# Kernel tuning notes

Measured on AMD Instinct MI355X. Metric: run time of the kernel, lower is better.

## Reference

```python
import jax, jax.numpy as jnp
import numpy as np

N = 40000
E = 640000
D_RNA = 1000
D_PROT = 300
H = 64      # hidden_channels
OUT = 32    # out_channels
HEADS = 4


def setup_inputs() -> dict:
    key = jax.random.key(0)
    ks = jax.random.split(key, 24)
    s = 0.05
    w = lambda k, shape: jax.random.normal(k, shape, jnp.float32) * s
    inp = {
        'x': jax.random.normal(ks[0], (N, D_RNA + D_PROT), jnp.float32),
        'edge_index': jax.random.randint(ks[1], (2, E), 0, N, jnp.int32),
        'input_dim_rna': D_RNA,
        # embeddings
        'W_rna': w(ks[2], (D_RNA, H)), 'b_rna': jnp.zeros((H,), jnp.float32),
        'W_prot': w(ks[3], (D_PROT, H)), 'b_prot': jnp.zeros((H,), jnp.float32),
        # GATConv1: in 2H=128 -> heads*H=256
        'W1s': w(ks[4], (2 * H, HEADS * H)), 'W1d': w(ks[5], (2 * H, HEADS * H)),
        'att1_s': w(ks[6], (HEADS, H)), 'att1_d': w(ks[7], (HEADS, H)),
        'bias1': jnp.zeros((HEADS * H,), jnp.float32),
        # lin1: 2H -> heads*H
        'Wl1': w(ks[8], (2 * H, HEADS * H)), 'bl1': jnp.zeros((HEADS * H,), jnp.float32),
        # GATConv2: in heads*H=256 -> heads*OUT=128
        'W2s': w(ks[9], (HEADS * H, HEADS * OUT)), 'W2d': w(ks[10], (HEADS * H, HEADS * OUT)),
        'att2_s': w(ks[11], (HEADS, OUT)), 'att2_d': w(ks[12], (HEADS, OUT)),
        'bias2': jnp.zeros((HEADS * OUT,), jnp.float32),
        # lin2: heads*H -> heads*OUT
        'Wl2': w(ks[13], (HEADS * H, HEADS * OUT)), 'bl2': jnp.zeros((HEADS * OUT,), jnp.float32),
    }
    return inp


def _gat(x_in, edge_index, Ws, Wd, att_s, att_d, bias, heads, ch):
    # PyG GATConv, bipartite weights, add_self_loops=False, concat=True, eval (no dropout)
    n = x_in.shape[0]
    src, dst = edge_index[0], edge_index[1]
    xs = (x_in @ Ws).reshape(n, heads, ch)   # source projection
    xd = (x_in @ Wd).reshape(n, heads, ch)   # destination projection
    a_s = jnp.einsum('nhc,hc->nh', xs, att_s)  # [N,H]
    a_d = jnp.einsum('nhc,hc->nh', xd, att_d)  # [N,H]
    e = jax.nn.leaky_relu(a_s[src] + a_d[dst], 0.2)          # [E,H]
    m = jax.lax.stop_gradient(jax.ops.segment_max(e, dst, num_segments=n))
    p = jnp.exp(e - m[dst])
    denom = jax.ops.segment_sum(p, dst, num_segments=n)       # [N,H]
    alpha = p / denom[dst]                                    # segment softmax over incoming edges
    msg = xs[src] * alpha[:, :, None]                         # [E,H,C]
    agg = jax.ops.segment_sum(msg, dst, num_segments=n)       # [N,H,C]
    return agg.reshape(n, heads * ch) + bias


def reference(x, edge_index, input_dim_rna, W_rna, b_rna, W_prot, b_prot,
              W1s, W1d, att1_s, att1_d, bias1, Wl1, bl1,
              W2s, W2d, att2_s, att2_d, bias2, Wl2, bl2):
    x_rna = x[:, :input_dim_rna] @ W_rna + b_rna
    x_prot = x[:, input_dim_rna:] @ W_prot + b_prot
    h = jnp.concatenate([x_rna, x_prot], axis=1)              # [N, 2H]
    h = _gat(h, edge_index, W1s, W1d, att1_s, att1_d, bias1, HEADS, H) + h @ Wl1 + bl1
    h = jax.nn.relu(h)
    out = _gat(h, edge_index, W2s, W2d, att2_s, att2_d, bias2, HEADS, OUT) + h @ Wl2 + bl2
    return out
```

## Files before the change

### kernel.cpp

```cpp
#include <hip/hip_runtime.h>
#include <hip/hip_bf16.h>
#include <stdint.h>


#define HEADS 4
#define CH1   64
#define CH2   32
#define HC1   256
#define HC2   128

static constexpr int D_RNA  = 1000;
static constexpr int D_PROT = 300;
static constexpr int D_IN   = 1300;
static constexpr int HDIM   = 128;

typedef __bf16 bf16x8 __attribute__((ext_vector_type(8)));
typedef float  f32x4  __attribute__((ext_vector_type(4)));
typedef unsigned short ushort;

__device__ __forceinline__ float lrelu(float x) { return x >= 0.f ? x : 0.2f * x; }
__device__ __forceinline__ float bf2f(unsigned int u16) {
  return __uint_as_float(u16 << 16);
}
__device__ __forceinline__ ushort f2bf(float f) {
  union { float f; unsigned int u; } x; x.f = f;
  unsigned int r = x.u + 0x7fffu + ((x.u >> 16) & 1u);
  return (ushort)(r >> 16);
}

__global__ void zero_i32(int* p, int n) {
  int i = blockIdx.x * 256 + threadIdx.x;
  if (i < n) p[i] = 0;
}

__global__ void hist_kernel(const int* __restrict__ dstv, int* __restrict__ deg, int E) {
  int i = blockIdx.x * 256 + threadIdx.x;
  if (i < E) atomicAdd(&deg[dstv[i]], 1);
}

__global__ void scan_kernel(const int* __restrict__ deg, int* __restrict__ off,
                            int* __restrict__ cur, int n) {
  __shared__ int s[1024];
  int tid = threadIdx.x;
  const int CHK = (n + 1023) / 1024;
  int base = tid * CHK;
  int sum = 0;
  for (int j = 0; j < CHK; ++j) {
    int i = base + j;
    if (i < n) sum += deg[i];
  }
  s[tid] = sum;
  __syncthreads();
  for (int o = 1; o < 1024; o <<= 1) {
    int t = (tid >= o) ? s[tid - o] : 0;
    __syncthreads();
    s[tid] += t;
    __syncthreads();
  }
  int run = s[tid] - sum;
  for (int j = 0; j < CHK; ++j) {
    int i = base + j;
    if (i < n) {
      off[i] = run; cur[i] = run;
      run += deg[i];
    }
  }
  if (tid == 1023) off[n] = s[1023];
}

__global__ void scatter_kernel(const int* __restrict__ srcv, const int* __restrict__ dstv,
                               int* __restrict__ cur, int* __restrict__ srcs, int E) {
  int i = blockIdx.x * 256 + threadIdx.x;
  if (i < E) {
    int d = dstv[i];
    int pos = atomicAdd(&cur[d], 1);
    srcs[pos] = srcv[i];
  }
}

__global__ void fold_att_kernel(const float* __restrict__ W1s, const float* __restrict__ W1d,
                                const float* __restrict__ at1s, const float* __restrict__ at1d,
                                const float* __restrict__ W2s, const float* __restrict__ W2d,
                                const float* __restrict__ at2s, const float* __restrict__ at2d,
                                float* v1s, float* v1d, float* v2s, float* v2d) {
  int tid = blockIdx.x * blockDim.x + threadIdx.x;
  int stride = gridDim.x * blockDim.x;
  for (int o = tid; o < HDIM * HEADS; o += stride) {
    int k = o >> 2, h = o & 3;
    float ss = 0.f, sd = 0.f;
    for (int c = 0; c < CH1; ++c) {
      ss += W1s[k * HC1 + h * CH1 + c] * at1s[h * CH1 + c];
      sd += W1d[k * HC1 + h * CH1 + c] * at1d[h * CH1 + c];
    }
    v1s[o] = ss; v1d[o] = sd;
  }
  for (int o = tid; o < HC1 * HEADS; o += stride) {
    int k = o >> 2, h = o & 3;
    float ss = 0.f, sd = 0.f;
    for (int c = 0; c < CH2; ++c) {
      ss += W2s[k * HC2 + h * CH2 + c] * at2s[h * CH2 + c];
      sd += W2d[k * HC2 + h * CH2 + c] * at2d[h * CH2 + c];
    }
    v2s[o] = ss; v2d[o] = sd;
  }
}

__global__ void convert_weights(const float* __restrict__ W_rna, const float* __restrict__ W_prot,
                                const float* __restrict__ W1s, const float* __restrict__ Wl1,
                                const float* __restrict__ W2s, const float* __restrict__ Wl2,
                                const float* __restrict__ b1, const float* __restrict__ bl1,
                                const float* __restrict__ b2, const float* __restrict__ bl2,
                                ushort* BTr, ushort* BTp, ushort* BT1, ushort* BT2,
                                float* biasL1, float* biasL2) {
  int tid = blockIdx.x * blockDim.x + threadIdx.x;
  int stride = gridDim.x * blockDim.x;
  for (int i = tid; i < 64 * 1024; i += stride) {
    int n = i >> 10, k = i & 1023;
    BTr[i] = (k < D_RNA) ? f2bf(W_rna[k * 64 + n]) : 0;
  }
  for (int i = tid; i < 64 * 320; i += stride) {
    int n = i / 320, k = i - n * 320;
    BTp[i] = (k < D_PROT) ? f2bf(W_prot[k * 64 + n]) : 0;
  }
  for (int i = tid; i < 512 * 128; i += stride) {
    int n = i >> 7, k = i & 127;
    BT1[i] = f2bf(n < 256 ? W1s[k * 256 + n] : Wl1[k * 256 + n - 256]);
  }
  for (int i = tid; i < 256 * 256; i += stride) {
    int n = i >> 8, k = i & 255;
    BT2[i] = f2bf(n < 128 ? W2s[k * 128 + n] : Wl2[k * 128 + n - 128]);
  }
  for (int i = tid; i < 512; i += stride) biasL1[i] = (i < 256) ? b1[i] : bl1[i - 256];
  for (int i = tid; i < 256; i += stride) biasL2[i] = (i < 128) ? b2[i] : bl2[i - 128];
}

#define LDK 72

__device__ __forceinline__ f32x4 mfma_bf16(bf16x8 a, bf16x8 b, f32x4 c) {
  return __builtin_amdgcn_mfma_f32_16x16x32_bf16(a, b, c, 0, 0, 0);
}

__launch_bounds__(256)
__global__ void embed_gemm(const float* __restrict__ x,
                           const ushort* __restrict__ BTr, const ushort* __restrict__ BTp,
                           const float* __restrict__ b_rna, const float* __restrict__ b_prot,
                           ushort* __restrict__ h0) {
  const bool prot = (blockIdx.x == 1);
  const int Kpad = prot ? 320 : 1024;
  const int acol = prot ? D_RNA : 0;
  const ushort* BT = prot ? BTp : BTr;
  const float* bias = prot ? b_prot : b_rna;
  const int r0 = blockIdx.y * 64;

  __shared__ ushort As[64 * LDK];
  __shared__ ushort Bs[64 * LDK];
  int tid = threadIdx.x;
  int wave = tid >> 6, lane = tid & 63;
  int quad = lane >> 4, lr = lane & 15;
  f32x4 acc[4];
#pragma unroll
  for (int c = 0; c < 4; ++c) acc[c] = (f32x4){0.f, 0.f, 0.f, 0.f};

  int srow = tid >> 2, skq = (tid & 3) * 16;
  const float* aprow = x + (size_t)(r0 + srow) * D_IN;
  const ushort* bprow = BT + (size_t)srow * Kpad;

  float4 fa[4];
  uint4 fb0, fb1;

  auto loadA = [&](int k0) {
#pragma unroll
    for (int q = 0; q < 4; ++q) {
      int kg = acol + k0 + skq + q * 4;
      fa[q] = (kg + 4 <= D_IN) ? *(const float4*)(aprow + kg)
                               : make_float4(0.f, 0.f, 0.f, 0.f);
    }
  };
  auto loadB = [&](int k0) {
    const ushort* bp = bprow + k0 + skq;
    fb0 = *(const uint4*)bp;
    fb1 = *(const uint4*)(bp + 8);
  };

  loadA(0);
  loadB(0);

  for (int k0 = 0; k0 < Kpad; k0 += 64) {
    {
      ushort tmp[16];
#pragma unroll
      for (int q = 0; q < 4; ++q) {
        tmp[q * 4 + 0] = f2bf(fa[q].x); tmp[q * 4 + 1] = f2bf(fa[q].y);
        tmp[q * 4 + 2] = f2bf(fa[q].z); tmp[q * 4 + 3] = f2bf(fa[q].w);
      }
      *(uint4*)&As[srow * LDK + skq] = *(const uint4*)&tmp[0];
      *(uint4*)&As[srow * LDK + skq + 8] = *(const uint4*)&tmp[8];
      *(uint4*)&Bs[srow * LDK + skq] = fb0;
      *(uint4*)&Bs[srow * LDK + skq + 8] = fb1;
    }
    __syncthreads();
    if (k0 + 64 < Kpad) {
      loadA(k0 + 64);
      loadB(k0 + 64);
    }
    int arow = wave * 16 + lr;
    bf16x8 a0 = *(const bf16x8*)&As[arow * LDK + quad * 8];
    bf16x8 a1 = *(const bf16x8*)&As[arow * LDK + 32 + quad * 8];
#pragma unroll
    for (int c = 0; c < 4; ++c) {
      bf16x8 b0 = *(const bf16x8*)&Bs[(c * 16 + lr) * LDK + quad * 8];
      bf16x8 b1 = *(const bf16x8*)&Bs[(c * 16 + lr) * LDK + 32 + quad * 8];
      acc[c] = mfma_bf16(a0, b0, acc[c]);
      acc[c] = mfma_bf16(a1, b1, acc[c]);
    }
    __syncthreads();
  }
  int colb = prot ? 64 : 0;
#pragma unroll
  for (int c = 0; c < 4; ++c) {
#pragma unroll
    for (int j = 0; j < 4; ++j) {
      int row = r0 + wave * 16 + quad * 4 + j;
      int col = c * 16 + lr;
      h0[(size_t)row * HDIM + colb + col] = f2bf(acc[c][j] + bias[col]);
    }
  }
}

__launch_bounds__(256)
__global__ void layer_gemm(const ushort* __restrict__ A, int K,
                           const ushort* __restrict__ BT, const float* __restrict__ bias,
                           ushort* __restrict__ out0, ushort* __restrict__ out1, int halfw) {
  const int cb = blockIdx.x * 64;
  const int r0 = blockIdx.y * 64;
  __shared__ ushort As[64 * LDK];
  __shared__ ushort Bs[64 * LDK];
  int tid = threadIdx.x;
  int wave = tid >> 6, lane = tid & 63;
  int quad = lane >> 4, lr = lane & 15;
  f32x4 acc[4];
#pragma unroll
  for (int c = 0; c < 4; ++c) acc[c] = (f32x4){0.f, 0.f, 0.f, 0.f};

  int srow = tid >> 2, skq = (tid & 3) * 16;
  const ushort* aprow = A + (size_t)(r0 + srow) * K;
  const ushort* bprow = BT + (size_t)(cb + srow) * K;

  uint4 fa0, fa1, fb0, fb1;
  auto loadAB = [&](int k0) {
    const ushort* ap = aprow + k0 + skq;
    const ushort* bp = bprow + k0 + skq;
    fa0 = *(const uint4*)ap;
    fa1 = *(const uint4*)(ap + 8);
    fb0 = *(const uint4*)bp;
    fb1 = *(const uint4*)(bp + 8);
  };

  loadAB(0);

  for (int k0 = 0; k0 < K; k0 += 64) {
    *(uint4*)&As[srow * LDK + skq] = fa0;
    *(uint4*)&As[srow * LDK + skq + 8] = fa1;
    *(uint4*)&Bs[srow * LDK + skq] = fb0;
    *(uint4*)&Bs[srow * LDK + skq + 8] = fb1;
    __syncthreads();
    if (k0 + 64 < K) loadAB(k0 + 64);
    int arow = wave * 16 + lr;
    bf16x8 a0 = *(const bf16x8*)&As[arow * LDK + quad * 8];
    bf16x8 a1 = *(const bf16x8*)&As[arow * LDK + 32 + quad * 8];
#pragma unroll
    for (int c = 0; c < 4; ++c) {
      bf16x8 b0 = *(const bf16x8*)&Bs[(c * 16 + lr) * LDK + quad * 8];
      bf16x8 b1 = *(const bf16x8*)&Bs[(c * 16 + lr) * LDK + 32 + quad * 8];
      acc[c] = mfma_bf16(a0, b0, acc[c]);
      acc[c] = mfma_bf16(a1, b1, acc[c]);
    }
    __syncthreads();
  }
#pragma unroll
  for (int c = 0; c < 4; ++c) {
#pragma unroll
    for (int j = 0; j < 4; ++j) {
      int row = r0 + wave * 16 + quad * 4 + j;
      int cg = cb + c * 16 + lr;
      ushort v = f2bf(acc[c][j] + bias[cg]);
      if (cg < halfw) out0[(size_t)row * halfw + cg] = v;
      else            out1[(size_t)row * halfw + cg - halfw] = v;
    }
  }
}

__launch_bounds__(256)
__global__ void attn_proj_kernel(const ushort* __restrict__ h, int K,
                                 const float* __restrict__ vs, const float* __restrict__ vd,
                                 float* __restrict__ a_s, float* __restrict__ a_d, int N) {
  extern __shared__ float lds[];
  float* VsT = lds;
  float* VdT = lds + 4 * K;
  for (int idx = threadIdx.x; idx < 4 * K; idx += 256) {
    int j = idx / K, k = idx - j * K;
    VsT[j * K + k] = vs[k * 4 + j];
    VdT[j * K + k] = vd[k * 4 + j];
  }
  __syncthreads();
  int wave = threadIdx.x >> 6, lane = threadIdx.x & 63;
  int n = blockIdx.x * 4 + wave;
  if (n >= N) return;
  float as[4] = {0.f, 0.f, 0.f, 0.f}, ad[4] = {0.f, 0.f, 0.f, 0.f};
  const ushort* hp = h + (size_t)n * K;
  for (int k = lane; k < K; k += 64) {
    float hv = bf2f(hp[k]);
#pragma unroll
    for (int j = 0; j < 4; ++j) {
      as[j] += hv * VsT[j * K + k];
      ad[j] += hv * VdT[j * K + k];
    }
  }
#pragma unroll
  for (int j = 0; j < 4; ++j) {
    for (int o = 32; o; o >>= 1) {
      as[j] += __shfl_xor(as[j], o);
      ad[j] += __shfl_xor(ad[j], o);
    }
  }
  if (lane == 0) {
#pragma unroll
    for (int j = 0; j < 4; ++j) {
      a_s[(size_t)n * 4 + j] = as[j];
      a_d[(size_t)n * 4 + j] = ad[j];
    }
  }
}

__launch_bounds__(256)
__global__ void edge_softmax_kernel(const int* __restrict__ off, const int* __restrict__ srcs,
                                    const float* __restrict__ a_s, const float* __restrict__ a_d,
                                    float* __restrict__ alpha, float* __restrict__ rden, int N) {
  int lane = threadIdx.x & 63;
  int wave = threadIdx.x >> 6;
  int g = lane >> 4, l = lane & 15;
  int n = (blockIdx.x * 4 + wave) * 4 + g;
  if (n >= N) return;
  int s0 = off[n], s1 = off[n + 1];
  float4 ad = *(const float4*)&a_d[(size_t)n * 4];
  float mx = -1e30f, my = -1e30f, mz = -1e30f, mw = -1e30f;
  for (int i = s0 + l; i < s1; i += 16) {
    float4 as = *(const float4*)&a_s[(size_t)srcs[i] * 4];
    mx = fmaxf(mx, lrelu(as.x + ad.x));
    my = fmaxf(my, lrelu(as.y + ad.y));
    mz = fmaxf(mz, lrelu(as.z + ad.z));
    mw = fmaxf(mw, lrelu(as.w + ad.w));
  }
#pragma unroll
  for (int o = 1; o < 16; o <<= 1) {
    mx = fmaxf(mx, __shfl_xor(mx, o));
    my = fmaxf(my, __shfl_xor(my, o));
    mz = fmaxf(mz, __shfl_xor(mz, o));
    mw = fmaxf(mw, __shfl_xor(mw, o));
  }
  float sx = 0.f, sy = 0.f, sz = 0.f, sw = 0.f;
  for (int i = s0 + l; i < s1; i += 16) {
    float4 as = *(const float4*)&a_s[(size_t)srcs[i] * 4];
    float4 p;
    p.x = expf(lrelu(as.x + ad.x) - mx);
    p.y = expf(lrelu(as.y + ad.y) - my);
    p.z = expf(lrelu(as.z + ad.z) - mz);
    p.w = expf(lrelu(as.w + ad.w) - mw);
    sx += p.x; sy += p.y; sz += p.z; sw += p.w;
    *(float4*)&alpha[(size_t)i * 4] = p;
  }
#pragma unroll
  for (int o = 1; o < 16; o <<= 1) {
    sx += __shfl_xor(sx, o);
    sy += __shfl_xor(sy, o);
    sz += __shfl_xor(sz, o);
    sw += __shfl_xor(sw, o);
  }
  if (l == 0) {
    float4 r;
    r.x = sx > 0.f ? 1.f / sx : 0.f;
    r.y = sy > 0.f ? 1.f / sy : 0.f;
    r.z = sz > 0.f ? 1.f / sz : 0.f;
    r.w = sw > 0.f ? 1.f / sw : 0.f;
    *(float4*)&rden[(size_t)n * 4] = r;
  }
}

template <int VEC>
__device__ __forceinline__ void load_bf(const ushort* p, float* out);
template <>
__device__ __forceinline__ void load_bf<4>(const ushort* p, float* out) {
  uint2 q = *(const uint2*)p;
  out[0] = bf2f(q.x & 0xffffu); out[1] = bf2f(q.x >> 16);
  out[2] = bf2f(q.y & 0xffffu); out[3] = bf2f(q.y >> 16);
}
template <>
__device__ __forceinline__ void load_bf<2>(const ushort* p, float* out) {
  unsigned int q = *(const unsigned int*)p;
  out[0] = bf2f(q & 0xffffu); out[1] = bf2f(q >> 16);
}

template <int CH, int VEC, bool RELU, bool OUT_BF16>
__launch_bounds__(256)
__global__ void aggregate_kernel(const int* __restrict__ off, const int* __restrict__ srcs,
                                 const float* __restrict__ alpha, const float* __restrict__ rden,
                                 const ushort* __restrict__ xs,
                                 const float* __restrict__ bias,
                                 const ushort* __restrict__ skip,
                                 void* __restrict__ outv, int N) {
  const int HC = 4 * CH;
  int wave = threadIdx.x >> 6, lane = threadIdx.x & 63;
  int n = blockIdx.x * 4 + wave;
  if (n >= N) return;
  int h = lane >> 4;
  int c = (lane & 15) * VEC;
  int i = off[n], end = off[n + 1];
  float acc[VEC];
#pragma unroll
  for (int v = 0; v < VEC; ++v) acc[v] = 0.f;
  for (; i + 2 <= end; i += 2) {
    int sA = srcs[i], sB = srcs[i + 1];
    float wA = alpha[(size_t)i * 4 + h];
    float wB = alpha[(size_t)(i + 1) * 4 + h];
    float xA[VEC], xB[VEC];
    load_bf<VEC>(xs + (size_t)sA * HC + h * CH + c, xA);
    load_bf<VEC>(xs + (size_t)sB * HC + h * CH + c, xB);
#pragma unroll
    for (int v = 0; v < VEC; ++v) acc[v] += wA * xA[v] + wB * xB[v];
  }
  if (i < end) {
    int sA = srcs[i];
    float wA = alpha[(size_t)i * 4 + h];
    float xA[VEC];
    load_bf<VEC>(xs + (size_t)sA * HC + h * CH + c, xA);
#pragma unroll
    for (int v = 0; v < VEC; ++v) acc[v] += wA * xA[v];
  }
  float r = rden[(size_t)n * 4 + h];
  size_t obase = (size_t)n * HC + h * CH + c;
  float sk[VEC];
  load_bf<VEC>(skip + obase, sk);
#pragma unroll
  for (int v = 0; v < VEC; ++v) {
    float val = acc[v] * r + bias[h * CH + c + v] + sk[v];
    if (RELU) val = fmaxf(val, 0.f);
    if (OUT_BF16) ((ushort*)outv)[obase + v] = f2bf(val);
    else          ((float*)outv)[obase + v] = val;
  }
}

extern "C" void kernel_launch(void* const* d_in, const int* in_sizes, int n_in,
                              void* d_out, int out_size, void* d_ws, size_t ws_size,
                              hipStream_t stream) {
  const float* x      = (const float*)d_in[0];
  const int*   ei     = (const int*)d_in[1];
  const float* W_rna  = (const float*)d_in[3];
  const float* b_rna  = (const float*)d_in[4];
  const float* W_prot = (const float*)d_in[5];
  const float* b_prot = (const float*)d_in[6];
  const float* W1s    = (const float*)d_in[7];
  const float* W1d    = (const float*)d_in[8];
  const float* at1s   = (const float*)d_in[9];
  const float* at1d   = (const float*)d_in[10];
  const float* bias1  = (const float*)d_in[11];
  const float* Wl1    = (const float*)d_in[12];
  const float* bl1    = (const float*)d_in[13];
  const float* W2s    = (const float*)d_in[14];
  const float* W2d    = (const float*)d_in[15];
  const float* at2s   = (const float*)d_in[16];
  const float* at2d   = (const float*)d_in[17];
  const float* bias2  = (const float*)d_in[18];
  const float* Wl2    = (const float*)d_in[19];
  const float* bl2    = (const float*)d_in[20];

  const int N = in_sizes[0] / D_IN;
  const int E = in_sizes[1] / 2;
  const int* srcv = ei;
  const int* dstv = ei + E;

  char* ws = (char*)d_ws;
  size_t o = 0;
  auto carve = [&](size_t bytes) {
    void* p = ws + o;
    o += (bytes + 255) & ~(size_t)255;
    return p;
  };
  int* deg    = (int*)carve((size_t)N * 4);
  int* offp   = (int*)carve((size_t)(N + 1) * 4);
  int* cur    = (int*)carve((size_t)N * 4);
  int* srcs   = (int*)carve((size_t)E * 4);
  float* v1s  = (float*)carve(HDIM * HEADS * 4);
  float* v1d  = (float*)carve(HDIM * HEADS * 4);
  float* v2s  = (float*)carve(HC1 * HEADS * 4);
  float* v2d  = (float*)carve(HC1 * HEADS * 4);
  float* a_s  = (float*)carve((size_t)N * 4 * 4);
  float* a_d  = (float*)carve((size_t)N * 4 * 4);
  float* rden = (float*)carve((size_t)N * 4 * 4);
  float* alpha = (float*)carve((size_t)E * 4 * 4);
  ushort* BTr = (ushort*)carve(64 * 1024 * 2);
  ushort* BTp = (ushort*)carve(64 * 320 * 2);
  ushort* BT1 = (ushort*)carve(512 * 128 * 2);
  ushort* BT2 = (ushort*)carve(256 * 256 * 2);
  float* biasL1 = (float*)carve(512 * 4);
  float* biasL2 = (float*)carve(256 * 4);
  ushort* h0  = (ushort*)carve((size_t)N * HDIM * 2);
  ushort* xs1 = (ushort*)carve((size_t)N * HC1 * 2);
  ushort* z1  = (ushort*)carve((size_t)N * HC1 * 2);
  ushort* h1  = (ushort*)carve((size_t)N * HC1 * 2);
  ushort* xs2 = h0;
  ushort* z2  = z1;
  float* out = (float*)d_out;

  zero_i32<<<(N + 255) / 256, 256, 0, stream>>>(deg, N);
  hist_kernel<<<(E + 255) / 256, 256, 0, stream>>>(dstv, deg, E);
  scan_kernel<<<1, 1024, 0, stream>>>(deg, offp, cur, N);
  scatter_kernel<<<(E + 255) / 256, 256, 0, stream>>>(srcv, dstv, cur, srcs, E);
  fold_att_kernel<<<8, 256, 0, stream>>>(W1s, W1d, at1s, at1d, W2s, W2d, at2s, at2d,
                                         v1s, v1d, v2s, v2d);
  convert_weights<<<256, 256, 0, stream>>>(W_rna, W_prot, W1s, Wl1, W2s, Wl2,
                                           bias1, bl1, bias2, bl2,
                                           BTr, BTp, BT1, BT2, biasL1, biasL2);
  embed_gemm<<<dim3(2, N / 64), 256, 0, stream>>>(x, BTr, BTp, b_rna, b_prot, h0);
  layer_gemm<<<dim3(8, N / 64), 256, 0, stream>>>(h0, HDIM, BT1, biasL1, xs1, z1, HC1);
  attn_proj_kernel<<<N / 4, 256, 8 * HDIM * 4, stream>>>(h0, HDIM, v1s, v1d, a_s, a_d, N);
  edge_softmax_kernel<<<N / 16, 256, 0, stream>>>(offp, srcs, a_s, a_d, alpha, rden, N);
  aggregate_kernel<CH1, 4, true, true><<<N / 4, 256, 0, stream>>>(offp, srcs, alpha, rden, xs1,
                                                                  bias1, z1, h1, N);
  layer_gemm<<<dim3(4, N / 64), 256, 0, stream>>>(h1, HC1, BT2, biasL2, xs2, z2, HC2);
  attn_proj_kernel<<<N / 4, 256, 8 * HC1 * 4, stream>>>(h1, HC1, v2s, v2d, a_s, a_d, N);
  edge_softmax_kernel<<<N / 16, 256, 0, stream>>>(offp, srcs, a_s, a_d, alpha, rden, N);
  aggregate_kernel<CH2, 2, false, false><<<N / 4, 256, 0, stream>>>(offp, srcs, alpha, rden, xs2,
                                                                    bias2, z2, out, N);
}
```

Baseline: 762.1 us.

## Split RNA embedding GEMM along K and widen K tile to 128

The RNA embedding GEMM is split into two K-halves computed by separate blocks, and their fp32 partial sums go to a workspace buffer. A new reduce kernel adds the halves plus bias into h0. The K step per iteration grows from 64 to 128, with the protein weights padded to 384. This balances work between the RNA and protein blocks and halves the number of barriers, at the cost of an extra launch, more shared memory per block and an extra fp32 round trip of about 20MB.

```diff
diff --git a/kernel.cpp b/kernel.cpp
--- a/kernel.cpp
+++ b/kernel.cpp
@@ -118,8 +118,8 @@
     int n = i >> 10, k = i & 1023;
     BTr[i] = (k < D_RNA) ? f2bf(W_rna[k * 64 + n]) : 0;
   }
-  for (int i = tid; i < 64 * 320; i += stride) {
-    int n = i / 320, k = i - n * 320;
+  for (int i = tid; i < 64 * 384; i += stride) {
+    int n = i / 384, k = i - n * 384;
     BTp[i] = (k < D_PROT) ? f2bf(W_prot[k * 64 + n]) : 0;
   }
   for (int i = tid; i < 512 * 128; i += stride) {
@@ -134,7 +134,8 @@
   for (int i = tid; i < 256; i += stride) biasL2[i] = (i < 128) ? b2[i] : bl2[i - 128];
 }
 
-#define LDK 72
+#define LDK  72
+#define LDKE 136
 
 __device__ __forceinline__ f32x4 mfma_bf16(bf16x8 a, bf16x8 b, f32x4 c) {
   return __builtin_amdgcn_mfma_f32_16x16x32_bf16(a, b, c, 0, 0, 0);
@@ -143,17 +144,20 @@
 __launch_bounds__(256)
 __global__ void embed_gemm(const float* __restrict__ x,
                            const ushort* __restrict__ BTr, const ushort* __restrict__ BTp,
-                           const float* __restrict__ b_rna, const float* __restrict__ b_prot,
-                           ushort* __restrict__ h0) {
-  const bool prot = (blockIdx.x == 1);
-  const int Kpad = prot ? 320 : 1024;
-  const int acol = prot ? D_RNA : 0;
-  const ushort* BT = prot ? BTp : BTr;
-  const float* bias = prot ? b_prot : b_rna;
+                           const float* __restrict__ b_prot,
+                           float* __restrict__ Ppart,
+                           ushort* __restrict__ h0, int N) {
+  const int part = blockIdx.x;
+  const bool prot = (part == 2);
+  const int Kstride = prot ? 384 : 1024;
+  const int kbase0  = prot ? 0 : part * 512;
+  const int Ktile   = prot ? 384 : 512;
+  const int acol    = prot ? D_RNA : 0;
+  const ushort* BT  = prot ? BTp : BTr;
   const int r0 = blockIdx.y * 64;
 
-  __shared__ ushort As[64 * LDK];
-  __shared__ ushort Bs[64 * LDK];
+  __shared__ ushort As[64 * LDKE];
+  __shared__ ushort Bs[64 * LDKE];
   int tid = threadIdx.x;
   int wave = tid >> 6, lane = tid & 63;
   int quad = lane >> 4, lr = lane & 15;
@@ -161,70 +165,102 @@
 #pragma unroll
   for (int c = 0; c < 4; ++c) acc[c] = (f32x4){0.f, 0.f, 0.f, 0.f};
 
-  int srow = tid >> 2, skq = (tid & 3) * 16;
-  const float* aprow = x + (size_t)(r0 + srow) * D_IN;
-  const ushort* bprow = BT + (size_t)srow * Kpad;
-
-  float4 fa[4];
-  uint4 fb0, fb1;
-
-  auto loadA = [&](int k0) {
-#pragma unroll
-    for (int q = 0; q < 4; ++q) {
-      int kg = acol + k0 + skq + q * 4;
-      fa[q] = (kg + 4 <= D_IN) ? *(const float4*)(aprow + kg)
+  int srow = tid >> 2, skq = (tid & 3) * 32;
+  const float* aprow = x + (size_t)(r0 + srow) * D_IN + acol;
+  const ushort* bprow = BT + (size_t)srow * Kstride;
+
+  float4 fa[8];
+  uint4 fb[4];
+  auto loadA = [&](int kb) {
+#pragma unroll
+    for (int q = 0; q < 8; ++q) {
+      int kg = acol + kb + skq + q * 4;
+      fa[q] = (kg + 4 <= D_IN) ? *(const float4*)(aprow + kb + skq + q * 4)
                                : make_float4(0.f, 0.f, 0.f, 0.f);
     }
   };
-  auto loadB = [&](int k0) {
-    const ushort* bp = bprow + k0 + skq;
-    fb0 = *(const uint4*)bp;
-    fb1 = *(const uint4*)(bp + 8);
+  auto loadB = [&](int kb) {
+    const ushort* bp = bprow + kb + skq;
+#pragma unroll
+    for (int q = 0; q < 4; ++q) fb[q] = *(const uint4*)(bp + q * 8);
   };
 
-  loadA(0);
-  loadB(0);
-
-  for (int k0 = 0; k0 < Kpad; k0 += 64) {
+  loadA(kbase0);
+  loadB(kbase0);
+
+  for (int k0 = 0; k0 < Ktile; k0 += 128) {
     {
-      ushort tmp[16];
-#pragma unroll
-      for (int q = 0; q < 4; ++q) {
+      ushort tmp[32];
+#pragma unroll
+      for (int q = 0; q < 8; ++q) {
         tmp[q * 4 + 0] = f2bf(fa[q].x); tmp[q * 4 + 1] = f2bf(fa[q].y);
         tmp[q * 4 + 2] = f2bf(fa[q].z); tmp[q * 4 + 3] = f2bf(fa[q].w);
       }
-      *(uint4*)&As[srow * LDK + skq] = *(const uint4*)&tmp[0];
-      *(uint4*)&As[srow * LDK + skq + 8] = *(const uint4*)&tmp[8];
-      *(uint4*)&Bs[srow * LDK + skq] = fb0;
-      *(uint4*)&Bs[srow * LDK + skq + 8] = fb1;
+#pragma unroll
+      for (int q = 0; q < 4; ++q) {
+        *(uint4*)&As[srow * LDKE + skq + q * 8] = *(const uint4*)&tmp[q * 8];
+        *(uint4*)&Bs[srow * LDKE + skq + q * 8] = fb[q];
+      }
     }
     __syncthreads();
-    if (k0 + 64 < Kpad) {
-      loadA(k0 + 64);
-      loadB(k0 + 64);
+    if (k0 + 128 < Ktile) {
+      loadA(kbase0 + k0 + 128);
+      loadB(kbase0 + k0 + 128);
     }
     int arow = wave * 16 + lr;
-    bf16x8 a0 = *(const bf16x8*)&As[arow * LDK + quad * 8];
-    bf16x8 a1 = *(const bf16x8*)&As[arow * LDK + 32 + quad * 8];
+    bf16x8 a[4];
+#pragma unroll
+    for (int ks = 0; ks < 4; ++ks)
+      a[ks] = *(const bf16x8*)&As[arow * LDKE + ks * 32 + quad * 8];
 #pragma unroll
     for (int c = 0; c < 4; ++c) {
-      bf16x8 b0 = *(const bf16x8*)&Bs[(c * 16 + lr) * LDK + quad * 8];
-      bf16x8 b1 = *(const bf16x8*)&Bs[(c * 16 + lr) * LDK + 32 + quad * 8];
-      acc[c] = mfma_bf16(a0, b0, acc[c]);
-      acc[c] = mfma_bf16(a1, b1, acc[c]);
+#pragma unroll
+      for (int ks = 0; ks < 4; ++ks) {
+        bf16x8 b = *(const bf16x8*)&Bs[(c * 16 + lr) * LDKE + ks * 32 + quad * 8];
+        acc[c] = mfma_bf16(a[ks], b, acc[c]);
+      }
     }
     __syncthreads();
   }
-  int colb = prot ? 64 : 0;
-#pragma unroll
-  for (int c = 0; c < 4; ++c) {
-#pragma unroll
-    for (int j = 0; j < 4; ++j) {
-      int row = r0 + wave * 16 + quad * 4 + j;
-      int col = c * 16 + lr;
-      h0[(size_t)row * HDIM + colb + col] = f2bf(acc[c][j] + bias[col]);
-    }
-  }
+
+  if (!prot) {
+    float* P = Ppart + (size_t)part * N * 64;
+#pragma unroll
+    for (int c = 0; c < 4; ++c) {
+#pragma unroll
+      for (int j = 0; j < 4; ++j) {
+        int row = r0 + wave * 16 + quad * 4 + j;
+        P[(size_t)row * 64 + c * 16 + lr] = acc[c][j];
+      }
+    }
+  } else {
+#pragma unroll
+    for (int c = 0; c < 4; ++c) {
+#pragma unroll
+      for (int j = 0; j < 4; ++j) {
+        int row = r0 + wave * 16 + quad * 4 + j;
+        int col = c * 16 + lr;
+        h0[(size_t)row * HDIM + 64 + col] = f2bf(acc[c][j] + b_prot[col]);
+      }
+    }
+  }
+}
+
+__launch_bounds__(256)
+__global__ void reduce_rna(const float* __restrict__ Ppart, const float* __restrict__ b_rna,
+                           ushort* __restrict__ h0, int N) {
+  int idx = blockIdx.x * 256 + threadIdx.x;
+  int row = idx >> 4, c4 = (idx & 15) * 4;
+  if (row >= N) return;
+  float4 a = *(const float4*)(Ppart + (size_t)row * 64 + c4);
+  float4 b = *(const float4*)(Ppart + (size_t)N * 64 + (size_t)row * 64 + c4);
+  float4 bias = *(const float4*)(b_rna + c4);
+  ushort o[4];
+  o[0] = f2bf(a.x + b.x + bias.x);
+  o[1] = f2bf(a.y + b.y + bias.y);
+  o[2] = f2bf(a.z + b.z + bias.z);
+  o[3] = f2bf(a.w + b.w + bias.w);
+  *(uint2*)&h0[(size_t)row * HDIM + c4] = *(const uint2*)o;
 }
 
 __launch_bounds__(256)
@@ -498,11 +534,12 @@
   float* rden = (float*)carve((size_t)N * 4 * 4);
   float* alpha = (float*)carve((size_t)E * 4 * 4);
   ushort* BTr = (ushort*)carve(64 * 1024 * 2);
-  ushort* BTp = (ushort*)carve(64 * 320 * 2);
+  ushort* BTp = (ushort*)carve(64 * 384 * 2);
   ushort* BT1 = (ushort*)carve(512 * 128 * 2);
   ushort* BT2 = (ushort*)carve(256 * 256 * 2);
   float* biasL1 = (float*)carve(512 * 4);
   float* biasL2 = (float*)carve(256 * 4);
+  float* Ppart = (float*)carve((size_t)2 * N * 64 * 4);
   ushort* h0  = (ushort*)carve((size_t)N * HDIM * 2);
   ushort* xs1 = (ushort*)carve((size_t)N * HC1 * 2);
   ushort* z1  = (ushort*)carve((size_t)N * HC1 * 2);
@@ -520,7 +557,8 @@
   convert_weights<<<256, 256, 0, stream>>>(W_rna, W_prot, W1s, Wl1, W2s, Wl2,
                                            bias1, bl1, bias2, bl2,
                                            BTr, BTp, BT1, BT2, biasL1, biasL2);
-  embed_gemm<<<dim3(2, N / 64), 256, 0, stream>>>(x, BTr, BTp, b_rna, b_prot, h0);
+  embed_gemm<<<dim3(3, N / 64), 256, 0, stream>>>(x, BTr, BTp, b_prot, Ppart, h0, N);
+  reduce_rna<<<(N * 16 + 255) / 256, 256, 0, stream>>>(Ppart, b_rna, h0, N);
   layer_gemm<<<dim3(8, N / 64), 256, 0, stream>>>(h0, HDIM, BT1, biasL1, xs1, z1, HC1);
   attn_proj_kernel<<<N / 4, 256, 8 * HDIM * 4, stream>>>(h0, HDIM, v1s, v1d, a_s, a_d, N);
   edge_softmax_kernel<<<N / 16, 256, 0, stream>>>(offp, srcs, a_s, a_d, alpha, rden, N);
```

Measured after the change: 834.7 us. +9.5%, slower.

## Fuse attention projections into GEMM and edge softmax into aggregation

Applied to the files above, without the earlier changes.

The attention logit projections are folded into the layer GEMM as an extra column block. Folded attention vectors are stored as bf16 hi/lo split pairs so the bf16 MFMA keeps near-fp32 precision. The separate edge-softmax kernel and its alpha/rden buffers are removed: the aggregate kernel now computes the per-head max and exp on the fly, normalising at the end. This cuts two launches per layer and the E×4 alpha write/read traffic, in exchange for recomputing gathered a_s values twice per edge and using the approximate __expf.

```diff
diff --git a/kernel.cpp b/kernel.cpp
--- a/kernel.cpp
+++ b/kernel.cpp
@@ -82,7 +82,7 @@
                                 const float* __restrict__ at1s, const float* __restrict__ at1d,
                                 const float* __restrict__ W2s, const float* __restrict__ W2d,
                                 const float* __restrict__ at2s, const float* __restrict__ at2d,
-                                float* v1s, float* v1d, float* v2s, float* v2d) {
+                                ushort* __restrict__ BTA1, ushort* __restrict__ BTA2) {
   int tid = blockIdx.x * blockDim.x + threadIdx.x;
   int stride = gridDim.x * blockDim.x;
   for (int o = tid; o < HDIM * HEADS; o += stride) {
@@ -92,7 +92,11 @@
       ss += W1s[k * HC1 + h * CH1 + c] * at1s[h * CH1 + c];
       sd += W1d[k * HC1 + h * CH1 + c] * at1d[h * CH1 + c];
     }
-    v1s[o] = ss; v1d[o] = sd;
+    ushort sh = f2bf(ss), dh = f2bf(sd);
+    BTA1[(0 + h) * HDIM + k] = sh;
+    BTA1[(4 + h) * HDIM + k] = f2bf(ss - bf2f(sh));
+    BTA1[(8 + h) * HDIM + k] = dh;
+    BTA1[(12 + h) * HDIM + k] = f2bf(sd - bf2f(dh));
   }
   for (int o = tid; o < HC1 * HEADS; o += stride) {
     int k = o >> 2, h = o & 3;
@@ -101,8 +105,14 @@
       ss += W2s[k * HC2 + h * CH2 + c] * at2s[h * CH2 + c];
       sd += W2d[k * HC2 + h * CH2 + c] * at2d[h * CH2 + c];
     }
-    v2s[o] = ss; v2d[o] = sd;
-  }
+    ushort sh = f2bf(ss), dh = f2bf(sd);
+    BTA2[(0 + h) * HC1 + k] = sh;
+    BTA2[(4 + h) * HC1 + k] = f2bf(ss - bf2f(sh));
+    BTA2[(8 + h) * HC1 + k] = dh;
+    BTA2[(12 + h) * HC1 + k] = f2bf(sd - bf2f(dh));
+  }
+  for (int i = tid; i < 48 * HDIM; i += stride) BTA1[16 * HDIM + i] = 0;
+  for (int i = tid; i < 48 * HC1; i += stride) BTA2[16 * HC1 + i] = 0;
 }
 
 __global__ void convert_weights(const float* __restrict__ W_rna, const float* __restrict__ W_prot,
@@ -230,8 +240,11 @@
 __launch_bounds__(256)
 __global__ void layer_gemm(const ushort* __restrict__ A, int K,
                            const ushort* __restrict__ BT, const float* __restrict__ bias,
-                           ushort* __restrict__ out0, ushort* __restrict__ out1, int halfw) {
-  const int cb = blockIdx.x * 64;
+                           ushort* __restrict__ out0, ushort* __restrict__ out1, int halfw,
+                           const ushort* __restrict__ BTA,
+                           float* __restrict__ a_s, float* __restrict__ a_d) {
+  const bool att = (blockIdx.x == gridDim.x - 1);
+  const int cb = att ? 0 : blockIdx.x * 64;
   const int r0 = blockIdx.y * 64;
   __shared__ ushort As[64 * LDK];
   __shared__ ushort Bs[64 * LDK];
@@ -244,7 +257,8 @@
 
   int srow = tid >> 2, skq = (tid & 3) * 16;
   const ushort* aprow = A + (size_t)(r0 + srow) * K;
-  const ushort* bprow = BT + (size_t)(cb + srow) * K;
+  const ushort* bprow = att ? (BTA + (size_t)srow * K)
+                            : (BT + (size_t)(cb + srow) * K);
 
   uint4 fa0, fa1, fb0, fb1;
   auto loadAB = [&](int k0) {
@@ -277,6 +291,17 @@
     }
     __syncthreads();
   }
+  if (att) {
+#pragma unroll
+    for (int j = 0; j < 4; ++j) {
+      int row = r0 + wave * 16 + quad * 4 + j;
+      float v0 = acc[0][j];
+      float sum = v0 + __shfl_xor(v0, 4);
+      if (lr < 4)                    a_s[(size_t)row * 4 + lr] = sum;
+      else if (lr >= 8 && lr < 12)   a_d[(size_t)row * 4 + (lr - 8)] = sum;
+    }
+    return;
+  }
 #pragma unroll
   for (int c = 0; c < 4; ++c) {
 #pragma unroll
@@ -287,102 +312,6 @@
       if (cg < halfw) out0[(size_t)row * halfw + cg] = v;
       else            out1[(size_t)row * halfw + cg - halfw] = v;
     }
-  }
-}
-
-__launch_bounds__(256)
-__global__ void attn_proj_kernel(const ushort* __restrict__ h, int K,
-                                 const float* __restrict__ vs, const float* __restrict__ vd,
-                                 float* __restrict__ a_s, float* __restrict__ a_d, int N) {
-  extern __shared__ float lds[];
-  float* VsT = lds;
-  float* VdT = lds + 4 * K;
-  for (int idx = threadIdx.x; idx < 4 * K; idx += 256) {
-    int j = idx / K, k = idx - j * K;
-    VsT[j * K + k] = vs[k * 4 + j];
-    VdT[j * K + k] = vd[k * 4 + j];
-  }
-  __syncthreads();
-  int wave = threadIdx.x >> 6, lane = threadIdx.x & 63;
-  int n = blockIdx.x * 4 + wave;
-  if (n >= N) return;
-  float as[4] = {0.f, 0.f, 0.f, 0.f}, ad[4] = {0.f, 0.f, 0.f, 0.f};
-  const ushort* hp = h + (size_t)n * K;
-  for (int k = lane; k < K; k += 64) {
-    float hv = bf2f(hp[k]);
-#pragma unroll
-    for (int j = 0; j < 4; ++j) {
-      as[j] += hv * VsT[j * K + k];
-      ad[j] += hv * VdT[j * K + k];
-    }
-  }
-#pragma unroll
-  for (int j = 0; j < 4; ++j) {
-    for (int o = 32; o; o >>= 1) {
-      as[j] += __shfl_xor(as[j], o);
-      ad[j] += __shfl_xor(ad[j], o);
-    }
-  }
-  if (lane == 0) {
-#pragma unroll
-    for (int j = 0; j < 4; ++j) {
-      a_s[(size_t)n * 4 + j] = as[j];
-      a_d[(size_t)n * 4 + j] = ad[j];
-    }
-  }
-}
-
-__launch_bounds__(256)
-__global__ void edge_softmax_kernel(const int* __restrict__ off, const int* __restrict__ srcs,
-                                    const float* __restrict__ a_s, const float* __restrict__ a_d,
-                                    float* __restrict__ alpha, float* __restrict__ rden, int N) {
-  int lane = threadIdx.x & 63;
-  int wave = threadIdx.x >> 6;
-  int g = lane >> 4, l = lane & 15;
-  int n = (blockIdx.x * 4 + wave) * 4 + g;
-  if (n >= N) return;
-  int s0 = off[n], s1 = off[n + 1];
-  float4 ad = *(const float4*)&a_d[(size_t)n * 4];
-  float mx = -1e30f, my = -1e30f, mz = -1e30f, mw = -1e30f;
-  for (int i = s0 + l; i < s1; i += 16) {
-    float4 as = *(const float4*)&a_s[(size_t)srcs[i] * 4];
-    mx = fmaxf(mx, lrelu(as.x + ad.x));
-    my = fmaxf(my, lrelu(as.y + ad.y));
-    mz = fmaxf(mz, lrelu(as.z + ad.z));
-    mw = fmaxf(mw, lrelu(as.w + ad.w));
-  }
-#pragma unroll
-  for (int o = 1; o < 16; o <<= 1) {
-    mx = fmaxf(mx, __shfl_xor(mx, o));
-    my = fmaxf(my, __shfl_xor(my, o));
-    mz = fmaxf(mz, __shfl_xor(mz, o));
-    mw = fmaxf(mw, __shfl_xor(mw, o));
-  }
-  float sx = 0.f, sy = 0.f, sz = 0.f, sw = 0.f;
-  for (int i = s0 + l; i < s1; i += 16) {
-    float4 as = *(const float4*)&a_s[(size_t)srcs[i] * 4];
-    float4 p;
-    p.x = expf(lrelu(as.x + ad.x) - mx);
-    p.y = expf(lrelu(as.y + ad.y) - my);
-    p.z = expf(lrelu(as.z + ad.z) - mz);
-    p.w = expf(lrelu(as.w + ad.w) - mw);
-    sx += p.x; sy += p.y; sz += p.z; sw += p.w;
-    *(float4*)&alpha[(size_t)i * 4] = p;
-  }
-#pragma unroll
-  for (int o = 1; o < 16; o <<= 1) {
-    sx += __shfl_xor(sx, o);
-    sy += __shfl_xor(sy, o);
-    sz += __shfl_xor(sz, o);
-    sw += __shfl_xor(sw, o);
-  }
-  if (l == 0) {
-    float4 r;
-    r.x = sx > 0.f ? 1.f / sx : 0.f;
-    r.y = sy > 0.f ? 1.f / sy : 0.f;
-    r.z = sz > 0.f ? 1.f / sz : 0.f;
-    r.w = sw > 0.f ? 1.f / sw : 0.f;
-    *(float4*)&rden[(size_t)n * 4] = r;
   }
 }
 
@@ -402,8 +331,8 @@
 
 template <int CH, int VEC, bool RELU, bool OUT_BF16>
 __launch_bounds__(256)
-__global__ void aggregate_kernel(const int* __restrict__ off, const int* __restrict__ srcs,
-                                 const float* __restrict__ alpha, const float* __restrict__ rden,
+__global__ void gat_fused_kernel(const int* __restrict__ off, const int* __restrict__ srcs,
+                                 const float* __restrict__ a_s, const float* __restrict__ a_d,
                                  const ushort* __restrict__ xs,
                                  const float* __restrict__ bias,
                                  const ushort* __restrict__ skip,
@@ -414,29 +343,47 @@
   if (n >= N) return;
   int h = lane >> 4;
   int c = (lane & 15) * VEC;
-  int i = off[n], end = off[n + 1];
+  int s0 = off[n], end = off[n + 1];
+  float adn = a_d[(size_t)n * 4 + h];
+
+  float m = -1e30f;
+  int i = s0;
+  for (; i + 4 <= end; i += 4) {
+    float e0 = a_s[(size_t)srcs[i] * 4 + h];
+    float e1 = a_s[(size_t)srcs[i + 1] * 4 + h];
+    float e2 = a_s[(size_t)srcs[i + 2] * 4 + h];
+    float e3 = a_s[(size_t)srcs[i + 3] * 4 + h];
+    m = fmaxf(m, fmaxf(fmaxf(lrelu(e0 + adn), lrelu(e1 + adn)),
+                       fmaxf(lrelu(e2 + adn), lrelu(e3 + adn))));
+  }
+  for (; i < end; ++i) m = fmaxf(m, lrelu(a_s[(size_t)srcs[i] * 4 + h] + adn));
+
+  float s = 0.f;
   float acc[VEC];
 #pragma unroll
   for (int v = 0; v < VEC; ++v) acc[v] = 0.f;
-  for (; i + 2 <= end; i += 2) {
+  for (i = s0; i + 2 <= end; i += 2) {
     int sA = srcs[i], sB = srcs[i + 1];
-    float wA = alpha[(size_t)i * 4 + h];
-    float wB = alpha[(size_t)(i + 1) * 4 + h];
+    float pA = __expf(lrelu(a_s[(size_t)sA * 4 + h] + adn) - m);
+    float pB = __expf(lrelu(a_s[(size_t)sB * 4 + h] + adn) - m);
+    s += pA + pB;
     float xA[VEC], xB[VEC];
     load_bf<VEC>(xs + (size_t)sA * HC + h * CH + c, xA);
     load_bf<VEC>(xs + (size_t)sB * HC + h * CH + c, xB);
 #pragma unroll
-    for (int v = 0; v < VEC; ++v) acc[v] += wA * xA[v] + wB * xB[v];
+    for (int v = 0; v < VEC; ++v) acc[v] += pA * xA[v] + pB * xB[v];
   }
   if (i < end) {
     int sA = srcs[i];
-    float wA = alpha[(size_t)i * 4 + h];
+    float pA = __expf(lrelu(a_s[(size_t)sA * 4 + h] + adn) - m);
+    s += pA;
     float xA[VEC];
     load_bf<VEC>(xs + (size_t)sA * HC + h * CH + c, xA);
 #pragma unroll
-    for (int v = 0; v < VEC; ++v) acc[v] += wA * xA[v];
-  }
-  float r = rden[(size_t)n * 4 + h];
+    for (int v = 0; v < VEC; ++v) acc[v] += pA * xA[v];
+  }
+
+  float r = s > 0.f ? 1.f / s : 0.f;
   size_t obase = (size_t)n * HC + h * CH + c;
   float sk[VEC];
   load_bf<VEC>(skip + obase, sk);
@@ -489,18 +436,14 @@
   int* offp   = (int*)carve((size_t)(N + 1) * 4);
   int* cur    = (int*)carve((size_t)N * 4);
   int* srcs   = (int*)carve((size_t)E * 4);
-  float* v1s  = (float*)carve(HDIM * HEADS * 4);
-  float* v1d  = (float*)carve(HDIM * HEADS * 4);
-  float* v2s  = (float*)carve(HC1 * HEADS * 4);
-  float* v2d  = (float*)carve(HC1 * HEADS * 4);
   float* a_s  = (float*)carve((size_t)N * 4 * 4);
   float* a_d  = (float*)carve((size_t)N * 4 * 4);
-  float* rden = (float*)carve((size_t)N * 4 * 4);
-  float* alpha = (float*)carve((size_t)E * 4 * 4);
   ushort* BTr = (ushort*)carve(64 * 1024 * 2);
   ushort* BTp = (ushort*)carve(64 * 320 * 2);
   ushort* BT1 = (ushort*)carve(512 * 128 * 2);
   ushort* BT2 = (ushort*)carve(256 * 256 * 2);
+  ushort* BTA1 = (ushort*)carve(64 * 128 * 2);
+  ushort* BTA2 = (ushort*)carve(64 * 256 * 2);
   float* biasL1 = (float*)carve(512 * 4);
   float* biasL2 = (float*)carve(256 * 4);
   ushort* h0  = (ushort*)carve((size_t)N * HDIM * 2);
@@ -516,19 +459,17 @@
   scan_kernel<<<1, 1024, 0, stream>>>(deg, offp, cur, N);
   scatter_kernel<<<(E + 255) / 256, 256, 0, stream>>>(srcv, dstv, cur, srcs, E);
   fold_att_kernel<<<8, 256, 0, stream>>>(W1s, W1d, at1s, at1d, W2s, W2d, at2s, at2d,
-                                         v1s, v1d, v2s, v2d);
+                                         BTA1, BTA2);
   convert_weights<<<256, 256, 0, stream>>>(W_rna, W_prot, W1s, Wl1, W2s, Wl2,
                                            bias1, bl1, bias2, bl2,
                                            BTr, BTp, BT1, BT2, biasL1, biasL2);
   embed_gemm<<<dim3(2, N / 64), 256, 0, stream>>>(x, BTr, BTp, b_rna, b_prot, h0);
-  layer_gemm<<<dim3(8, N / 64), 256, 0, stream>>>(h0, HDIM, BT1, biasL1, xs1, z1, HC1);
-  attn_proj_kernel<<<N / 4, 256, 8 * HDIM * 4, stream>>>(h0, HDIM, v1s, v1d, a_s, a_d, N);
-  edge_softmax_kernel<<<N / 16, 256, 0, stream>>>(offp, srcs, a_s, a_d, alpha, rden, N);
-  aggregate_kernel<CH1, 4, true, true><<<N / 4, 256, 0, stream>>>(offp, srcs, alpha, rden, xs1,
+  layer_gemm<<<dim3(9, N / 64), 256, 0, stream>>>(h0, HDIM, BT1, biasL1, xs1, z1, HC1,
+                                                  BTA1, a_s, a_d);
+  gat_fused_kernel<CH1, 4, true, true><<<N / 4, 256, 0, stream>>>(offp, srcs, a_s, a_d, xs1,
                                                                   bias1, z1, h1, N);
-  layer_gemm<<<dim3(4, N / 64), 256, 0, stream>>>(h1, HC1, BT2, biasL2, xs2, z2, HC2);
-  attn_proj_kernel<<<N / 4, 256, 8 * HC1 * 4, stream>>>(h1, HC1, v2s, v2d, a_s, a_d, N);
-  edge_softmax_kernel<<<N / 16, 256, 0, stream>>>(offp, srcs, a_s, a_d, alpha, rden, N);
-  aggregate_kernel<CH2, 2, false, false><<<N / 4, 256, 0, stream>>>(offp, srcs, alpha, rden, xs2,
+  layer_gemm<<<dim3(5, N / 64), 256, 0, stream>>>(h1, HC1, BT2, biasL2, xs2, z2, HC2,
+                                                  BTA2, a_s, a_d);
+  gat_fused_kernel<CH2, 2, false, false><<<N / 4, 256, 0, stream>>>(offp, srcs, a_s, a_d, xs2,
                                                                     bias2, z2, out, N);
 }
```

Result: faster. 706.7 us (-7.3%).
